# Kernel optimization log

Measured on AMD Instinct MI355X. Metric: run time of the kernel, lower is better.

## Reference

```python
import jax, jax.numpy as jnp
import numpy as np

BN_EPS = 1e-5


def _gcn(x, A, W, gamma, beta):
    # x: [B,N,Cin], A: [B,N,N] -> [B,N,Cout]; BatchNorm1d over (B,N) per channel (train-mode batch stats)
    h = jnp.einsum('bnm,bmc->bnc', A, x @ W)
    mu = h.mean(axis=(0, 1))
    var = h.var(axis=(0, 1))
    h = (h - mu) * jax.lax.rsqrt(var + BN_EPS) * gamma + beta
    return jax.nn.relu(h)  # dropout is identity (drop_prob=0 / eval)


def _ppige(x, A, W0, g0, b0, W_res, g_res, b_res):
    h = _gcn(x, A, W0, g0, b0)
    for i in range(W_res.shape[0]):  # residual GCN stack (num_GCN-1 layers)
        h = _gcn(h, A, W_res[i], g_res[i], b_res[i]) + h
    return h


def _gge(x, w1, b1, w2, b2):
    return jax.nn.relu(jax.nn.relu(x @ w1 + b1) @ w2 + b2)


def _gaga(G, h):
    # G: [B,N,H], h: [B,H]
    att = jax.nn.softmax(jnp.einsum('bnh,bh->bn', G, h), axis=-1)
    return jnp.einsum('bnh,bn->bh', G, att)


def _led(ea, eb, conv_w, conv_b, p1_w, p1_b, p2_w, p2_b):
    # ea, eb: [B, 2H]; Conv1d(2H->2H, k=1) over length-2 axis then MaxPool1d(2)
    stacked = jnp.stack([ea, eb], axis=-1)  # [B, 2H, 2]
    conv = jnp.einsum('oc,bct->bot', conv_w, stacked) + conv_b[None, :, None]
    cnn_x = conv.max(axis=-1)  # [B, 2H]
    x = jax.nn.relu(jnp.concatenate([cnn_x, ea - eb], axis=1) @ p1_w + p1_b)
    return x @ p2_w + p2_b


def setup_inputs() -> dict:
    key = jax.random.key(0)
    ks = jax.random.split(key, 24)
    Bs, N, PPI_in, H, F_in = 8, 2048, 512, 256, 1024
    n_res = 3  # num_GCN - 1
    s = 0.02
    adjA = jax.random.uniform(ks[0], (Bs, N, N), jnp.float32)
    adjB = jax.random.uniform(ks[1], (Bs, N, N), jnp.float32)
    adjA = adjA / adjA.sum(-1, keepdims=True)  # row-normalized for numerical sanity
    adjB = adjB / adjB.sum(-1, keepdims=True)
    return {
        'a': jax.random.normal(ks[2], (Bs, F_in), jnp.float32),
        'bio_a': jax.random.normal(ks[3], (Bs, N, PPI_in), jnp.float32),
        'A': adjA,
        'b': jax.random.normal(ks[4], (Bs, F_in), jnp.float32),
        'bio_b': jax.random.normal(ks[5], (Bs, N, PPI_in), jnp.float32),
        'B': adjB,
        'W0': jax.random.normal(ks[6], (PPI_in, H), jnp.float32) * s,
        'gamma0': jnp.ones((H,), jnp.float32),
        'beta0': jnp.zeros((H,), jnp.float32),
        'W_res': jax.random.normal(ks[7], (n_res, H, H), jnp.float32) * s,
        'gamma_res': jnp.ones((n_res, H), jnp.float32),
        'beta_res': jnp.zeros((n_res, H), jnp.float32),
        'g1_w': jax.random.normal(ks[8], (F_in, 128), jnp.float32) * s,
        'g1_b': jnp.zeros((128,), jnp.float32),
        'g2_w': jax.random.normal(ks[9], (128, H), jnp.float32) * s,
        'g2_b': jnp.zeros((H,), jnp.float32),
        'conv_w': jax.random.normal(ks[10], (2 * H, 2 * H), jnp.float32) * s,
        'conv_b': jnp.zeros((2 * H,), jnp.float32),
        'p1_w': jax.random.normal(ks[11], (4 * H, H), jnp.float32) * s,
        'p1_b': jnp.zeros((H,), jnp.float32),
        'p2_w': jax.random.normal(ks[12], (H, 2), jnp.float32) * s,
        'p2_b': jnp.zeros((2,), jnp.float32),
    }


def reference(a, bio_a, A, b, bio_b, B, W0, gamma0, beta0, W_res, gamma_res, beta_res,
              g1_w, g1_b, g2_w, g2_b, conv_w, conv_b, p1_w, p1_b, p2_w, p2_b):
    Ga = _ppige(bio_a, A, W0, gamma0, beta0, W_res, gamma_res, beta_res)
    Gb = _ppige(bio_b, B, W0, gamma0, beta0, W_res, gamma_res, beta_res)
    ha = _gge(a, g1_w, g1_b, g2_w, g2_b)
    hb = _gge(b, g1_w, g1_b, g2_w, g2_b)
    ea = jnp.concatenate([ha, _gaga(Ga, ha)], axis=-1)
    eb = jnp.concatenate([hb, _gaga(Gb, hb)], axis=-1)
    logits = _led(ea, eb, conv_w, conv_b, p1_w, p1_b, p2_w, p2_b)
    return jax.nn.log_softmax(logits, axis=-1)
```

## Files before the change

kernel.cpp:

```cpp
#include <hip/hip_runtime.h>
#include <hip/hip_bf16.h>
#include <cstdint>

typedef unsigned short u16;
typedef __bf16 bf16x8 __attribute__((ext_vector_type(8)));
typedef float f32x4 __attribute__((ext_vector_type(4)));

typedef __attribute__((address_space(1))) const void* gas_ptr;
typedef __attribute__((address_space(3))) void* las_ptr;

__device__ __forceinline__ u16 f2bf(float f) {
  union { __hip_bfloat16 h; u16 u; } v;
  v.h = __float2bfloat16(f);
  return v.u;
}
__device__ __forceinline__ float bf2f(u16 u) {
  union { unsigned int i; float f; } v;
  v.i = ((unsigned int)u) << 16;
  return v.f;
}

__device__ __forceinline__ void gload16(const u16* g, u16* l) {
  __builtin_amdgcn_global_load_lds((gas_ptr)g, (las_ptr)l, 16, 0, 0);
}

__global__ __launch_bounds__(256) void k_prep_weights(const float* __restrict__ W0,
                                                      const float* __restrict__ Wres,
                                                      u16* __restrict__ W0t,
                                                      u16* __restrict__ Wrt) {
  __shared__ float tile[32][33];
  int y = blockIdx.y;
  const float* src; u16* dst; int R, r0;
  if (y < 16) { src = W0; dst = W0t; R = 512; r0 = y * 32; }
  else {
    int i = (y - 16) >> 3;
    src = Wres + i * 65536; dst = Wrt + i * 65536; R = 256; r0 = ((y - 16) & 7) * 32;
  }
  const int C = 256;
  int c0 = blockIdx.x * 32;
  int tx = threadIdx.x & 31, ty = threadIdx.x >> 5;
#pragma unroll
  for (int i = 0; i < 4; ++i) {
    int r = ty + i * 8;
    tile[r][tx] = src[(long)(r0 + r) * C + c0 + tx];
  }
  __syncthreads();
#pragma unroll
  for (int i = 0; i < 4; ++i) {
    int c = ty + i * 8;
    dst[(long)(c0 + c) * R + r0 + tx] = f2bf(tile[tx][c]);
  }
}

template<int EPI, int SWZ, int CVT>
__global__ __launch_bounds__(256) void k_gemm(
    const u16* __restrict__ A, int lda, long sA,
    const float* __restrict__ Afa, const float* __restrict__ Afb,
    long splitRow, int ldaf, long zrows, u16* __restrict__ AbfOut,
    const u16* __restrict__ Bt, int ldb, long sB,
    u16* __restrict__ C, int ldc, long sC,
    u16* __restrict__ PtOut, int ldpt,
    float* __restrict__ stats, int K) {
  __shared__ __align__(16) u16 smem[4][8192];
  __shared__ float cs[256];
  const int tid = threadIdx.x;
  const int lane = tid & 63;
  const int wid = tid >> 6;
  const int wm = wid >> 1, wn = wid & 1;

  int bx = blockIdx.x, by = blockIdx.y, bz = blockIdx.z;
  if (SWZ == 1) {
    int lin = bx + 16 * by + 32 * bz;
    int swz = (lin & 7) * 64 + (lin >> 3);
    bx = swz & 15; by = (swz >> 4) & 1; bz = swz >> 5;
  } else if (SWZ == 2) {
    int t = bx; bx = by; by = t;
  }
  const long m0 = (long)bx * 128, n0 = (long)by * 128;
  const int z = bz;
  const u16* Ab = A + (long)z * sA;
  const u16* Btb = Bt + (long)z * sB;

  const int rsub = lane >> 3;
  const int swzcol = ((lane & 7) ^ rsub) * 8;
  const long a_row = m0 + wid * 32 + rsub;
  const long b_row = n0 + wid * 32 + rsub;

  if (EPI == 0) cs[tid] = 0.f;

  const f32x4 zero = {0.f, 0.f, 0.f, 0.f};
  f32x4 acc[4][4];
#pragma unroll
  for (int i = 0; i < 4; ++i)
#pragma unroll
    for (int j = 0; j < 4; ++j) acc[i][j] = zero;

  const int fr = lane & 15;
  const int kgrp = lane >> 4;
  const int swz_rd = lane & 7;
  const int nk = K >> 6;

  float4 rgf[8];

  auto stageA = [&](int buf, int k0) {
#pragma unroll
    for (int i = 0; i < 4; ++i)
      gload16(Ab + (a_row + i * 8) * (long)lda + (k0 + swzcol),
              &smem[buf][(wid * 32 + i * 8) * 64]);
  };
  auto stageB = [&](int buf, int k0) {
#pragma unroll
    for (int i = 0; i < 4; ++i)
      gload16(Btb + (b_row + i * 8) * (long)ldb + (k0 + swzcol),
              &smem[2 + buf][(wid * 32 + i * 8) * 64]);
  };
  auto loadA = [&](int k0) {
#pragma unroll
    for (int i = 0; i < 4; ++i) {
      long R = (long)z * zrows + a_row + i * 8;
      const float* sp = (R < splitRow ? Afa + R * (long)ldaf
                                      : Afb + (R - splitRow) * (long)ldaf) + k0 + swzcol;
      rgf[i * 2] = *reinterpret_cast<const float4*>(sp);
      rgf[i * 2 + 1] = *reinterpret_cast<const float4*>(sp + 4);
    }
  };
  auto writeA = [&](int buf, int k0) {
#pragma unroll
    for (int i = 0; i < 4; ++i) {
      union { u16 u[8]; uint4 qq; } o;
      o.u[0] = f2bf(rgf[i*2].x);   o.u[1] = f2bf(rgf[i*2].y);
      o.u[2] = f2bf(rgf[i*2].z);   o.u[3] = f2bf(rgf[i*2].w);
      o.u[4] = f2bf(rgf[i*2+1].x); o.u[5] = f2bf(rgf[i*2+1].y);
      o.u[6] = f2bf(rgf[i*2+1].z); o.u[7] = f2bf(rgf[i*2+1].w);
      if (AbfOut && by == 0) {
        long R = (long)z * zrows + a_row + i * 8;
        *reinterpret_cast<uint4*>(AbfOut + R * (long)ldaf + k0 + swzcol) = o.qq;
      }
      *reinterpret_cast<uint4*>(&smem[buf][(wid * 32 + i * 8) * 64 + lane * 8]) = o.qq;
    }
  };
  auto compute = [&](const u16* Asb, const u16* Bsb) {
#pragma unroll
    for (int ks = 0; ks < 2; ++ks) {
      bf16x8 af[4], bfv[4];
#pragma unroll
      for (int f = 0; f < 4; ++f) {
        int cA = (ks * 4 + kgrp) ^ swz_rd;
        af[f]  = *reinterpret_cast<const bf16x8*>(&Asb[(wm * 64 + f * 16 + fr) * 64 + cA * 8]);
        bfv[f] = *reinterpret_cast<const bf16x8*>(&Bsb[(wn * 64 + f * 16 + fr) * 64 + cA * 8]);
      }
#pragma unroll
      for (int mf = 0; mf < 4; ++mf)
#pragma unroll
        for (int nf = 0; nf < 4; ++nf)
          acc[mf][nf] = __builtin_amdgcn_mfma_f32_16x16x32_bf16(af[mf], bfv[nf], acc[mf][nf], 0, 0, 0);
    }
  };

  if constexpr (CVT) {
    loadA(0); stageB(0, 0); writeA(0, 0);
    for (int t = 0; t < nk; ++t) {
      int cur = t & 1, nxt = cur ^ 1;
      if (t + 1 < nk) {
        loadA((t + 1) * 64);
        stageB(nxt, (t + 1) * 64);
        asm volatile("s_waitcnt vmcnt(12) lgkmcnt(0)" ::: "memory");
      } else {
        asm volatile("s_waitcnt vmcnt(0) lgkmcnt(0)" ::: "memory");
      }
      __builtin_amdgcn_s_barrier();
      __builtin_amdgcn_sched_barrier(0);
      compute(smem[cur], smem[2 + cur]);
      if (t + 1 < nk) writeA(nxt, (t + 1) * 64);
      asm volatile("s_waitcnt lgkmcnt(0)" ::: "memory");
      __builtin_amdgcn_s_barrier();
    }
  } else {
    stageA(0, 0); stageB(0, 0);
    for (int t = 0; t < nk; ++t) {
      int cur = t & 1, nxt = cur ^ 1;
      if (t + 1 < nk) {
        stageA(nxt, (t + 1) * 64);
        stageB(nxt, (t + 1) * 64);
        asm volatile("s_waitcnt vmcnt(8) lgkmcnt(0)" ::: "memory");
      } else {
        asm volatile("s_waitcnt vmcnt(0) lgkmcnt(0)" ::: "memory");
      }
      __builtin_amdgcn_s_barrier();
      __builtin_amdgcn_sched_barrier(0);
      compute(smem[cur], smem[2 + cur]);
      asm volatile("s_waitcnt lgkmcnt(0)" ::: "memory");
      __builtin_amdgcn_s_barrier();
    }
  }

  if (EPI == 0) {
    u16* Cb = C + (long)z * sC;
    const int side = z >> 3;
#pragma unroll
    for (int mf = 0; mf < 4; ++mf) {
      long mrow = m0 + wm * 64 + mf * 16 + kgrp * 4;
#pragma unroll
      for (int nf = 0; nf < 4; ++nf) {
        long ncol = n0 + wn * 64 + nf * 16 + fr;
#pragma unroll
        for (int r = 0; r < 4; ++r)
          Cb[(mrow + r) * ldc + ncol] = f2bf(acc[mf][nf][r]);
      }
    }
#pragma unroll
    for (int nf = 0; nf < 4; ++nf) {
      int cl = wn * 64 + nf * 16 + fr;
      float s = 0.f, q = 0.f;
#pragma unroll
      for (int mf = 0; mf < 4; ++mf)
#pragma unroll
        for (int r = 0; r < 4; ++r) { float v = acc[mf][nf][r]; s += v; q += v * v; }
      atomicAdd(&cs[cl], s);
      atomicAdd(&cs[128 + cl], q);
    }
    __syncthreads();
    if (tid < 128) atomicAdd(&stats[side * 512 + n0 + tid], cs[tid]);
    else           atomicAdd(&stats[side * 512 + 256 + n0 + (tid - 128)], cs[tid]);
  } else {
    u16* Ts = &smem[0][0];
#pragma unroll
    for (int mf = 0; mf < 4; ++mf)
#pragma unroll
      for (int nf = 0; nf < 4; ++nf) {
        int nl = wn * 64 + nf * 16 + fr;
        int ml = wm * 64 + mf * 16 + kgrp * 4;
#pragma unroll
        for (int r = 0; r < 4; ++r)
          Ts[nl * 136 + ml + r] = f2bf(acc[mf][nf][r]);
      }
    __syncthreads();
    int n = tid >> 1, half = tid & 1;
    const u16* sp = Ts + n * 136 + half * 64;
    u16* dp = PtOut + (long)(n0 + n) * ldpt + m0 + half * 64;
#pragma unroll
    for (int j = 0; j < 8; ++j)
      reinterpret_cast<uint4*>(dp)[j] = reinterpret_cast<const uint4*>(sp)[j];
  }
}

__global__ __launch_bounds__(256) void k_bn_apply(const ushort4* __restrict__ u4,
                                                  ushort4* __restrict__ h4,
                                                  const float* __restrict__ statsL,
                                                  const float* __restrict__ gamma,
                                                  const float* __restrict__ beta, int res) {
  long i = (long)blockIdx.x * 256 + threadIdx.x;
  int side = (int)(i >> 20);
  int c0 = (int)(i & 63) * 4;
  const float* st = statsL + side * 512;
  ushort4 uv = u4[i];
  float vp[4] = { bf2f(uv.x), bf2f(uv.y), bf2f(uv.z), bf2f(uv.w) };
  float rp[4];
#pragma unroll
  for (int j = 0; j < 4; ++j) {
    int c = c0 + j;
    float mu = st[c] * (1.f / 16384.f);
    float var = st[256 + c] * (1.f / 16384.f) - mu * mu;
    float sc = gamma[c] * rsqrtf(var + 1e-5f);
    float sh = beta[c] - mu * sc;
    rp[j] = fmaxf(vp[j] * sc + sh, 0.f);
  }
  if (res) {
    ushort4 hv = h4[i];
    rp[0] += bf2f(hv.x); rp[1] += bf2f(hv.y); rp[2] += bf2f(hv.z); rp[3] += bf2f(hv.w);
  }
  ushort4 o;
  o.x = f2bf(rp[0]); o.y = f2bf(rp[1]); o.z = f2bf(rp[2]); o.w = f2bf(rp[3]);
  h4[i] = o;
}

__global__ __launch_bounds__(256) void k_gge(const float* __restrict__ in_a,
                                             const float* __restrict__ in_b,
                                             const float* __restrict__ w1, const float* __restrict__ b1,
                                             const float* __restrict__ w2, const float* __restrict__ b2,
                                             float* __restrict__ ha) {
  __shared__ float av[1024];
  __shared__ float hid[128];
  int bx = blockIdx.x, t = threadIdx.x;
  const float* ap = ((bx >> 3) ? in_b : in_a) + (bx & 7) * 1024;
  for (int i = t; i < 1024; i += 256) av[i] = ap[i];
  __syncthreads();
  if (t < 128) {
    float s = b1[t];
    for (int c = 0; c < 1024; ++c) s += av[c] * w1[c * 128 + t];
    hid[t] = fmaxf(s, 0.f);
  }
  __syncthreads();
  float s = b2[t];
  for (int c = 0; c < 128; ++c) s += hid[c] * w2[c * 256 + t];
  ha[bx * 256 + t] = fmaxf(s, 0.f);
}

__global__ __launch_bounds__(256) void k_gaga_scores(const u16* __restrict__ h,
                                                     const float* __restrict__ ha,
                                                     float* __restrict__ sc) {
  __shared__ __align__(16) float has[256];
  int bx = blockIdx.x;
  has[threadIdx.x] = ha[bx * 256 + threadIdx.x];
  __syncthreads();
  const u16* G = h + (long)bx * 524288;
  int wv = threadIdx.x >> 6, lane = threadIdx.x & 63;
  float4 h4 = reinterpret_cast<const float4*>(has)[lane];
  for (int i = 0; i < 32; ++i) {
    int n = blockIdx.y * 128 + wv * 32 + i;
    ushort4 v = reinterpret_cast<const ushort4*>(G + (long)n * 256)[lane];
    float d = bf2f(v.x) * h4.x + bf2f(v.y) * h4.y + bf2f(v.z) * h4.z + bf2f(v.w) * h4.w;
#pragma unroll
    for (int o2 = 32; o2 > 0; o2 >>= 1) d += __shfl_down(d, o2);
    if (lane == 0) sc[bx * 2048 + n] = d;
  }
}

__global__ __launch_bounds__(256) void k_softmax2048(const float* __restrict__ sc, float* __restrict__ att) {
  __shared__ float red[256];
  int b = blockIdx.x, t = threadIdx.x;
  const float* s = sc + b * 2048;
  float* o = att + b * 2048;
  float v[8];
  float m = -1e30f;
#pragma unroll
  for (int i = 0; i < 8; ++i) { v[i] = s[t + i * 256]; m = fmaxf(m, v[i]); }
  red[t] = m; __syncthreads();
  for (int o2 = 128; o2 > 0; o2 >>= 1) { if (t < o2) red[t] = fmaxf(red[t], red[t + o2]); __syncthreads(); }
  m = red[0]; __syncthreads();
  float sum = 0.f;
#pragma unroll
  for (int i = 0; i < 8; ++i) { v[i] = expf(v[i] - m); sum += v[i]; }
  red[t] = sum; __syncthreads();
  for (int o2 = 128; o2 > 0; o2 >>= 1) { if (t < o2) red[t] += red[t + o2]; __syncthreads(); }
  float inv = 1.f / red[0];
#pragma unroll
  for (int i = 0; i < 8; ++i) o[t + i * 256] = v[i] * inv;
}

__global__ __launch_bounds__(256) void k_gaga_out(const u16* __restrict__ h,
                                                  const float* __restrict__ att,
                                                  float* __restrict__ ga) {
  __shared__ float atts[128];
  int bx = blockIdx.x, n0 = blockIdx.y * 128, c = threadIdx.x;
  if (threadIdx.x < 128) atts[threadIdx.x] = att[bx * 2048 + n0 + threadIdx.x];
  __syncthreads();
  const u16* base = h + (long)bx * 524288 + (long)n0 * 256 + c;
  float s = 0.f;
#pragma unroll 4
  for (int i = 0; i < 128; ++i) s += bf2f(base[(long)i * 256]) * atts[i];
  atomicAdd(&ga[bx * 256 + c], s);
}

__global__ __launch_bounds__(512) void k_led_conv(const float* __restrict__ ha, const float* __restrict__ ga,
                                                  const float* __restrict__ hb, const float* __restrict__ gb,
                                                  const float* __restrict__ cw, const float* __restrict__ cb,
                                                  float* __restrict__ cnn, float* __restrict__ diff) {
  __shared__ float ea[8][512], eb[8][512];
  int t = threadIdx.x;
  for (int i = t; i < 4096; i += 512) {
    int b = i >> 9, c = i & 511;
    float va = (c < 256) ? ha[b * 256 + c] : ga[b * 256 + c - 256];
    float vb = (c < 256) ? hb[b * 256 + c] : gb[b * 256 + c - 256];
    ea[b][c] = va; eb[b][c] = vb;
    if (blockIdx.x == 0) diff[i] = va - vb;
  }
  __syncthreads();
  int o = blockIdx.x * 64 + (t >> 3), b = t & 7;
  const float* wr = cw + (long)o * 512;
  float s0 = cb[o], s1 = s0;
  for (int c = 0; c < 512; ++c) { float w = wr[c]; s0 += w * ea[b][c]; s1 += w * eb[b][c]; }
  cnn[b * 512 + o] = fmaxf(s0, s1);
}

__global__ __launch_bounds__(256) void k_led_p1(const float* __restrict__ cnn, const float* __restrict__ diff,
                                                const float* __restrict__ w, const float* __restrict__ pb,
                                                float* __restrict__ x) {
  __shared__ float cat[8][1024];
  int t = threadIdx.x;
  for (int i = t; i < 8192; i += 256) {
    int b = i >> 10, c = i & 1023;
    cat[b][c] = (c < 512) ? cnn[b * 512 + c] : diff[b * 512 + c - 512];
  }
  __syncthreads();
  int o = blockIdx.x * 32 + (t >> 3), b = t & 7;
  float s = pb[o];
  for (int c = 0; c < 1024; ++c) s += cat[b][c] * w[c * 256 + o];
  x[b * 256 + o] = fmaxf(s, 0.f);
}

__global__ __launch_bounds__(64) void k_led_final(const float* __restrict__ x,
                                                  const float* __restrict__ p2w, const float* __restrict__ p2b,
                                                  float* __restrict__ out) {
  __shared__ float lg[16];
  int t = threadIdx.x;
  if (t < 16) {
    int b = t >> 1, j = t & 1;
    float s = p2b[j];
    for (int c = 0; c < 256; ++c) s += x[b * 256 + c] * p2w[c * 2 + j];
    lg[t] = s;
  }
  __syncthreads();
  if (t < 8) {
    float l0 = lg[t * 2], l1 = lg[t * 2 + 1];
    float m = fmaxf(l0, l1);
    float lse = m + logf(expf(l0 - m) + expf(l1 - m));
    out[t * 2] = l0 - lse;
    out[t * 2 + 1] = l1 - lse;
  }
}

extern "C" void kernel_launch(void* const* d_in, const int* in_sizes, int n_in,
                              void* d_out, int out_size, void* d_ws, size_t ws_size,
                              hipStream_t stream) {
  const float* in_a   = (const float*)d_in[0];
  const float* bio_a  = (const float*)d_in[1];
  const float* adj_a  = (const float*)d_in[2];
  const float* in_b   = (const float*)d_in[3];
  const float* bio_b  = (const float*)d_in[4];
  const float* adj_b  = (const float*)d_in[5];
  const float* W0     = (const float*)d_in[6];
  const float* gamma0 = (const float*)d_in[7];
  const float* beta0  = (const float*)d_in[8];
  const float* W_res  = (const float*)d_in[9];
  const float* g_res  = (const float*)d_in[10];
  const float* b_res  = (const float*)d_in[11];
  const float* g1_w   = (const float*)d_in[12];
  const float* g1_b   = (const float*)d_in[13];
  const float* g2_w   = (const float*)d_in[14];
  const float* g2_b   = (const float*)d_in[15];
  const float* conv_w = (const float*)d_in[16];
  const float* conv_b = (const float*)d_in[17];
  const float* p1_w   = (const float*)d_in[18];
  const float* p1_b   = (const float*)d_in[19];
  const float* p2_w   = (const float*)d_in[20];
  const float* p2_b   = (const float*)d_in[21];
  float* out = (float*)d_out;

  char* ws = (char*)d_ws;
  size_t off = 0;
  auto alloc = [&](size_t bytes) {
    char* p = ws + off;
    off += (bytes + 255) & ~(size_t)255;
    return p;
  };
  u16*   Abf   = (u16*)  alloc(67108864ull * 2);
  u16*   Pt    = (u16*)  alloc(8388608ull * 2);
  u16*   ubf   = (u16*)  alloc(8388608ull * 2);
  u16*   hbf   = (u16*)  alloc(8388608ull * 2);
  u16*   W0t   = (u16*)  alloc(131072ull * 2);
  u16*   Wrt   = (u16*)  alloc(196608ull * 2);
  float* stats = (float*)alloc(4096 * 4);
  float* gabuf = (float*)alloc(4096 * 4);
  float* hav   = (float*)alloc(4096 * 4);
  float* scb   = (float*)alloc(32768 * 4);
  float* attb  = (float*)alloc(32768 * 4);
  float* cnn   = (float*)alloc(4096 * 4);
  float* diff  = (float*)alloc(4096 * 4);
  float* xbuf  = (float*)alloc(2048 * 4);

  k_prep_weights<<<dim3(8, 40), 256, 0, stream>>>(W0, W_res, W0t, Wrt);
  (void)hipMemsetAsync(stats, 0, 32768, stream);

  for (int layer = 0; layer < 4; ++layer) {
    float* statsL = stats + layer * 1024;
    const float* gm = (layer == 0) ? gamma0 : (g_res + (layer - 1) * 256);
    const float* bt = (layer == 0) ? beta0 : (b_res + (layer - 1) * 256);

    if (layer == 0) {
      k_gemm<1, 2, 1><<<dim3(2, 256, 1), 256, 0, stream>>>(
          nullptr, 0, 0, bio_a, bio_b, 16384L, 512, 0, nullptr,
          W0t, 512, 0, nullptr, 0, 0, Pt, 32768, nullptr, 512);
      k_gemm<0, 1, 1><<<dim3(16, 2, 16), 256, 0, stream>>>(
          nullptr, 0, 0, adj_a, adj_b, 16384L, 2048, 2048, Abf,
          Pt, 32768, 2048, ubf, 256, 524288L, nullptr, 0, statsL, 2048);
    } else {
      const u16* Wt = Wrt + (layer - 1) * 65536;
      k_gemm<1, 2, 0><<<dim3(2, 256, 1), 256, 0, stream>>>(
          hbf, 256, 0, nullptr, nullptr, 0, 0, 0, nullptr,
          Wt, 256, 0, nullptr, 0, 0, Pt, 32768, nullptr, 256);
      k_gemm<0, 1, 0><<<dim3(16, 2, 16), 256, 0, stream>>>(
          Abf, 2048, 4194304L, nullptr, nullptr, 0, 0, 0, nullptr,
          Pt, 32768, 2048, ubf, 256, 524288L, nullptr, 0, statsL, 2048);
    }
    k_bn_apply<<<8192, 256, 0, stream>>>((const ushort4*)ubf, (ushort4*)hbf,
                                         statsL, gm, bt, layer ? 1 : 0);
  }

  k_gge<<<16, 256, 0, stream>>>(in_a, in_b, g1_w, g1_b, g2_w, g2_b, hav);
  k_gaga_scores<<<dim3(16, 16), 256, 0, stream>>>(hbf, hav, scb);
  k_softmax2048<<<16, 256, 0, stream>>>(scb, attb);
  k_gaga_out<<<dim3(16, 16), 256, 0, stream>>>(hbf, attb, gabuf);

  k_led_conv<<<8, 512, 0, stream>>>(hav, gabuf, hav + 2048, gabuf + 2048, conv_w, conv_b, cnn, diff);
  k_led_p1<<<8, 256, 0, stream>>>(cnn, diff, p1_w, p1_b, xbuf);
  k_led_final<<<1, 64, 0, stream>>>(xbuf, p2_w, p2_b, out);
}
```

Baseline: 551.3 us.

## Widen GEMM tiles to 128x256 with 512-thread blocks covering full N

The GEMM kernel now uses 8 waves (512 threads) and a 128x256 output tile, so one block covers the full 256-wide N dimension. The A operand is loaded once per block instead of twice, which removes the duplicate fp32 adjacency reads and conversions in layer 0. The tile swizzle is generalized to group blocks across the grid. The cost is fewer blocks (256 per GEMM), more LDS per block (about 98KB), which lowers occupancy, and more B traffic per block.

```diff
diff --git a/kernel.cpp b/kernel.cpp
--- a/kernel.cpp
+++ b/kernel.cpp
@@ -52,8 +52,8 @@
   }
 }
 
-template<int EPI, int SWZ, int CVT>
-__global__ __launch_bounds__(256) void k_gemm(
+template<int EPI, int CVT>
+__global__ __launch_bounds__(512) void k_gemm(
     const u16* __restrict__ A, int lda, long sA,
     const float* __restrict__ Afa, const float* __restrict__ Afb,
     long splitRow, int ldaf, long zrows, u16* __restrict__ AbfOut,
@@ -61,30 +61,31 @@
     u16* __restrict__ C, int ldc, long sC,
     u16* __restrict__ PtOut, int ldpt,
     float* __restrict__ stats, int K) {
-  __shared__ __align__(16) u16 smem[4][8192];
-  __shared__ float cs[256];
+  __shared__ __align__(16) u16 smem[49152];
+  __shared__ float cs[512];
   const int tid = threadIdx.x;
   const int lane = tid & 63;
   const int wid = tid >> 6;
-  const int wm = wid >> 1, wn = wid & 1;
-
-  int bx = blockIdx.x, by = blockIdx.y, bz = blockIdx.z;
-  if (SWZ == 1) {
-    int lin = bx + 16 * by + 32 * bz;
-    int swz = (lin & 7) * 64 + (lin >> 3);
-    bx = swz & 15; by = (swz >> 4) & 1; bz = swz >> 5;
-  } else if (SWZ == 2) {
-    int t = bx; bx = by; by = t;
-  }
-  const long m0 = (long)bx * 128, n0 = (long)by * 128;
+  const int wm = wid >> 2, wn = wid & 3;
+
+  int bx = blockIdx.x, bz = blockIdx.z;
+  {
+    int nx = gridDim.x;
+    int tiles = nx * gridDim.z;
+    int lin = bx + nx * bz;
+    int chunk = tiles >> 3;
+    int swz = (lin & 7) * chunk + (lin >> 3);
+    bx = swz % nx; bz = swz / nx;
+  }
+  const long m0 = (long)bx * 128;
   const int z = bz;
   const u16* Ab = A + (long)z * sA;
   const u16* Btb = Bt + (long)z * sB;
 
   const int rsub = lane >> 3;
   const int swzcol = ((lane & 7) ^ rsub) * 8;
-  const long a_row = m0 + wid * 32 + rsub;
-  const long b_row = n0 + wid * 32 + rsub;
+  const long a_row = m0 + wid * 16 + rsub;
+  const int b_row = wid * 32 + rsub;
 
   if (EPI == 0) cs[tid] = 0.f;
 
@@ -100,23 +101,23 @@
   const int swz_rd = lane & 7;
   const int nk = K >> 6;
 
-  float4 rgf[8];
-
-  auto stageA = [&](int buf, int k0) {
+  float4 rgf[4];
+
+  auto stageA = [&](int bufofs, int k0) {
+#pragma unroll
+    for (int i = 0; i < 2; ++i)
+      gload16(Ab + (a_row + i * 8) * (long)lda + (k0 + swzcol),
+              &smem[bufofs + (wid * 16 + i * 8) * 64]);
+  };
+  auto stageB = [&](int bufofs, int k0) {
 #pragma unroll
     for (int i = 0; i < 4; ++i)
-      gload16(Ab + (a_row + i * 8) * (long)lda + (k0 + swzcol),
-              &smem[buf][(wid * 32 + i * 8) * 64]);
-  };
-  auto stageB = [&](int buf, int k0) {
-#pragma unroll
-    for (int i = 0; i < 4; ++i)
-      gload16(Btb + (b_row + i * 8) * (long)ldb + (k0 + swzcol),
-              &smem[2 + buf][(wid * 32 + i * 8) * 64]);
+      gload16(Btb + (long)(b_row + i * 8) * ldb + (k0 + swzcol),
+              &smem[bufofs + (wid * 32 + i * 8) * 64]);
   };
   auto loadA = [&](int k0) {
 #pragma unroll
-    for (int i = 0; i < 4; ++i) {
+    for (int i = 0; i < 2; ++i) {
       long R = (long)z * zrows + a_row + i * 8;
       const float* sp = (R < splitRow ? Afa + R * (long)ldaf
                                       : Afb + (R - splitRow) * (long)ldaf) + k0 + swzcol;
@@ -124,19 +125,19 @@
       rgf[i * 2 + 1] = *reinterpret_cast<const float4*>(sp + 4);
     }
   };
-  auto writeA = [&](int buf, int k0) {
-#pragma unroll
-    for (int i = 0; i < 4; ++i) {
+  auto writeA = [&](int bufofs, int k0) {
+#pragma unroll
+    for (int i = 0; i < 2; ++i) {
       union { u16 u[8]; uint4 qq; } o;
       o.u[0] = f2bf(rgf[i*2].x);   o.u[1] = f2bf(rgf[i*2].y);
       o.u[2] = f2bf(rgf[i*2].z);   o.u[3] = f2bf(rgf[i*2].w);
       o.u[4] = f2bf(rgf[i*2+1].x); o.u[5] = f2bf(rgf[i*2+1].y);
       o.u[6] = f2bf(rgf[i*2+1].z); o.u[7] = f2bf(rgf[i*2+1].w);
-      if (AbfOut && by == 0) {
+      if (AbfOut) {
         long R = (long)z * zrows + a_row + i * 8;
         *reinterpret_cast<uint4*>(AbfOut + R * (long)ldaf + k0 + swzcol) = o.qq;
       }
-      *reinterpret_cast<uint4*>(&smem[buf][(wid * 32 + i * 8) * 64 + lane * 8]) = o.qq;
+      *reinterpret_cast<uint4*>(&smem[bufofs + (wid * 16 + i * 8) * 64 + lane * 8]) = o.qq;
     }
   };
   auto compute = [&](const u16* Asb, const u16* Bsb) {
@@ -158,37 +159,37 @@
   };
 
   if constexpr (CVT) {
-    loadA(0); stageB(0, 0); writeA(0, 0);
+    loadA(0); stageB(16384, 0); writeA(0, 0);
     for (int t = 0; t < nk; ++t) {
       int cur = t & 1, nxt = cur ^ 1;
       if (t + 1 < nk) {
         loadA((t + 1) * 64);
-        stageB(nxt, (t + 1) * 64);
-        asm volatile("s_waitcnt vmcnt(12) lgkmcnt(0)" ::: "memory");
+        stageB(16384 + nxt * 16384, (t + 1) * 64);
+        asm volatile("s_waitcnt vmcnt(8) lgkmcnt(0)" ::: "memory");
       } else {
         asm volatile("s_waitcnt vmcnt(0) lgkmcnt(0)" ::: "memory");
       }
       __builtin_amdgcn_s_barrier();
       __builtin_amdgcn_sched_barrier(0);
-      compute(smem[cur], smem[2 + cur]);
-      if (t + 1 < nk) writeA(nxt, (t + 1) * 64);
+      compute(&smem[cur * 8192], &smem[16384 + cur * 16384]);
+      if (t + 1 < nk) writeA(nxt * 8192, (t + 1) * 64);
       asm volatile("s_waitcnt lgkmcnt(0)" ::: "memory");
       __builtin_amdgcn_s_barrier();
     }
   } else {
-    stageA(0, 0); stageB(0, 0);
+    stageA(0, 0); stageB(16384, 0);
     for (int t = 0; t < nk; ++t) {
       int cur = t & 1, nxt = cur ^ 1;
       if (t + 1 < nk) {
-        stageA(nxt, (t + 1) * 64);
-        stageB(nxt, (t + 1) * 64);
-        asm volatile("s_waitcnt vmcnt(8) lgkmcnt(0)" ::: "memory");
+        stageA(nxt * 8192, (t + 1) * 64);
+        stageB(16384 + nxt * 16384, (t + 1) * 64);
+        asm volatile("s_waitcnt vmcnt(6) lgkmcnt(0)" ::: "memory");
       } else {
         asm volatile("s_waitcnt vmcnt(0) lgkmcnt(0)" ::: "memory");
       }
       __builtin_amdgcn_s_barrier();
       __builtin_amdgcn_sched_barrier(0);
-      compute(smem[cur], smem[2 + cur]);
+      compute(&smem[cur * 8192], &smem[16384 + cur * 16384]);
       asm volatile("s_waitcnt lgkmcnt(0)" ::: "memory");
       __builtin_amdgcn_s_barrier();
     }
@@ -202,7 +203,7 @@
       long mrow = m0 + wm * 64 + mf * 16 + kgrp * 4;
 #pragma unroll
       for (int nf = 0; nf < 4; ++nf) {
-        long ncol = n0 + wn * 64 + nf * 16 + fr;
+        int ncol = wn * 64 + nf * 16 + fr;
 #pragma unroll
         for (int r = 0; r < 4; ++r)
           Cb[(mrow + r) * ldc + ncol] = f2bf(acc[mf][nf][r]);
@@ -217,13 +218,12 @@
 #pragma unroll
         for (int r = 0; r < 4; ++r) { float v = acc[mf][nf][r]; s += v; q += v * v; }
       atomicAdd(&cs[cl], s);
-      atomicAdd(&cs[128 + cl], q);
+      atomicAdd(&cs[256 + cl], q);
     }
     __syncthreads();
-    if (tid < 128) atomicAdd(&stats[side * 512 + n0 + tid], cs[tid]);
-    else           atomicAdd(&stats[side * 512 + 256 + n0 + (tid - 128)], cs[tid]);
+    atomicAdd(&stats[side * 512 + tid], cs[tid]);
   } else {
-    u16* Ts = &smem[0][0];
+    u16* Ts = &smem[0];
 #pragma unroll
     for (int mf = 0; mf < 4; ++mf)
 #pragma unroll
@@ -237,7 +237,7 @@
     __syncthreads();
     int n = tid >> 1, half = tid & 1;
     const u16* sp = Ts + n * 136 + half * 64;
-    u16* dp = PtOut + (long)(n0 + n) * ldpt + m0 + half * 64;
+    u16* dp = PtOut + (long)n * ldpt + m0 + half * 64;
 #pragma unroll
     for (int j = 0; j < 8; ++j)
       reinterpret_cast<uint4*>(dp)[j] = reinterpret_cast<const uint4*>(sp)[j];
@@ -468,18 +468,18 @@
     const float* bt = (layer == 0) ? beta0 : (b_res + (layer - 1) * 256);
 
     if (layer == 0) {
-      k_gemm<1, 2, 1><<<dim3(2, 256, 1), 256, 0, stream>>>(
+      k_gemm<1, 1><<<dim3(256, 1, 1), 512, 0, stream>>>(
           nullptr, 0, 0, bio_a, bio_b, 16384L, 512, 0, nullptr,
           W0t, 512, 0, nullptr, 0, 0, Pt, 32768, nullptr, 512);
-      k_gemm<0, 1, 1><<<dim3(16, 2, 16), 256, 0, stream>>>(
+      k_gemm<0, 1><<<dim3(16, 1, 16), 512, 0, stream>>>(
           nullptr, 0, 0, adj_a, adj_b, 16384L, 2048, 2048, Abf,
           Pt, 32768, 2048, ubf, 256, 524288L, nullptr, 0, statsL, 2048);
     } else {
       const u16* Wt = Wrt + (layer - 1) * 65536;
-      k_gemm<1, 2, 0><<<dim3(2, 256, 1), 256, 0, stream>>>(
+      k_gemm<1, 0><<<dim3(256, 1, 1), 512, 0, stream>>>(
           hbf, 256, 0, nullptr, nullptr, 0, 0, 0, nullptr,
           Wt, 256, 0, nullptr, 0, 0, Pt, 32768, nullptr, 256);
-      k_gemm<0, 1, 0><<<dim3(16, 2, 16), 256, 0, stream>>>(
+      k_gemm<0, 0><<<dim3(16, 1, 16), 512, 0, stream>>>(
           Abf, 2048, 4194304L, nullptr, nullptr, 0, 0, 0, nullptr,
           Pt, 32768, 2048, ubf, 256, 524288L, nullptr, 0, statsL, 2048);
     }
```

Result: no change. 561.0 us (+1.8%).
